# Kernel tuning notes

Measured on AMD Instinct MI355X. Metric: run time of the kernel, lower is better.

Reference implementation:

```python
import jax, jax.numpy as jnp
import numpy as np

D_MODEL, D_INNER, D_STATE, DT_RANK, USERS = 2560, 5120, 16, 160, 32

def setup_inputs() -> dict:
    key = jax.random.key(0)
    ks = jax.random.split(key, 16)
    s = lambda k, shp, sc=0.02: (jax.random.normal(k, shp, dtype=jnp.float32) * sc)
    return {
        "x": jax.random.normal(ks[0], (1, 1, USERS, D_MODEL), dtype=jnp.float32),
        "w_in_ssm": s(ks[1], (D_MODEL, D_INNER)),
        "w_in_mlp": s(ks[2], (D_MODEL, D_INNER)),
        "w_out": s(ks[3], (D_INNER, D_MODEL)),
        "conv_w": s(ks[4], (4, D_INNER), 0.5),
        "conv_b": s(ks[5], (D_INNER,), 0.1),
        "conv_state1": jax.random.normal(ks[6], (1, 1, USERS, D_INNER), dtype=jnp.float32),
        "conv_state2": jax.random.normal(ks[7], (1, 1, USERS, D_INNER), dtype=jnp.float32),
        "conv_state3": jax.random.normal(ks[8], (1, 1, USERS, D_INNER), dtype=jnp.float32),
        "x_proj_w": s(ks[9], (D_INNER, DT_RANK + 2 * D_STATE)),
        "dt_proj_w": s(ks[10], (DT_RANK, D_INNER)),
        "dt_proj_b": s(ks[11], (D_INNER,), 0.1),
        "A_log": jax.random.uniform(ks[12], (D_INNER, D_STATE), dtype=jnp.float32),
        "D_param": s(ks[13], (D_INNER,), 1.0),
        "ssm_state": jax.random.normal(ks[14], (USERS, D_INNER, D_STATE), dtype=jnp.float32) * 0.1,
    }

def reference(x, w_in_ssm, w_in_mlp, w_out, conv_w, conv_b,
              conv_state1, conv_state2, conv_state3,
              x_proj_w, dt_proj_w, dt_proj_b, A_log, D_param, ssm_state):
    xb = x.reshape(USERS, D_MODEL)                       # [U, d_model]
    xs = xb @ w_in_ssm                                    # [U, d_inner] (newest conv tap)
    # 4-tap depthwise causal conv via shifted state buffer (unrolled in original)
    taps = (conv_state1.reshape(USERS, D_INNER),
            conv_state2.reshape(USERS, D_INNER),
            conv_state3.reshape(USERS, D_INNER),
            xs)
    c = taps[0] * conv_w[0] + taps[1] * conv_w[1] + taps[2] * conv_w[2] + taps[3] * conv_w[3] + conv_b
    c = jax.nn.silu(c)                                    # [U, d_inner]
    # selective SSM single-step update
    x_dbl = c @ x_proj_w                                  # [U, dt_rank + 2*d_state]
    dt = jax.nn.softplus(x_dbl[:, :DT_RANK] @ dt_proj_w + dt_proj_b)   # [U, d_inner]
    B = x_dbl[:, DT_RANK:DT_RANK + D_STATE]               # [U, d_state]
    C = x_dbl[:, DT_RANK + D_STATE:]                      # [U, d_state]
    A = -jnp.exp(A_log)                                   # [d_inner, d_state]
    dA = jnp.exp(dt[:, :, None] * A[None])                # [U, d_inner, d_state]
    new_state = ssm_state * dA + (dt * c)[:, :, None] * B[:, None, :]
    y = jnp.einsum("uds,us->ud", new_state, C) + D_param * c           # [U, d_inner]
    res = xb @ w_in_mlp                                   # gate branch (no extra silu, per source)
    out = (y * res) @ w_out                               # [U, d_model]
    return out.reshape(1, 1, USERS, D_MODEL)
```

## Files before the change

kernel.cpp:

```cpp
#include <hip/hip_runtime.h>
#include <hip/hip_bf16.h>
#include <cstdint>
#include <cstddef>

#define U   32
#define DM  2560
#define DI  5120
#define DS  16
#define RNK 160
#define XD  192
#define KC1 8
#define KC4 32

typedef __attribute__((ext_vector_type(8)))  short bf16x8;
typedef __attribute__((ext_vector_type(16))) float f32x16;

__device__ __forceinline__ unsigned int pkbf(float a, float b) {
  __hip_bfloat162 h = __float22bfloat162_rn(make_float2(a, b));
  union { __hip_bfloat162 h; unsigned int u; } v; v.h = h; return v.u;
}
__device__ __forceinline__ unsigned short f2bfu(float f) {
  __hip_bfloat16 h = __float2bfloat16(f);
  union { __hip_bfloat16 h; unsigned short u; } v; v.h = h; return v.u;
}
__device__ __forceinline__ float bf2f(unsigned int s) {
  union { float f; unsigned int u; } v; v.u = s << 16; return v.f;
}

__device__ __forceinline__ void gl_lds16(const float* g, float* l) {
  __builtin_amdgcn_global_load_lds(
      (const __attribute__((address_space(1))) unsigned int*)g,
      (__attribute__((address_space(3))) unsigned int*)l,
      16, 0, 0);
}

template<int LDW, int SLAB>
__global__ __launch_bounds__(256, 3) void skinny_dma(
    const float* __restrict__ A, int lda,
    const float* __restrict__ W0, const float* __restrict__ W1,
    unsigned short* __restrict__ part)
{
  constexpr int NS = SLAB / 16;
  __shared__ float        wbuf[2][16][256];
  __shared__ unsigned int albuf[NS][64][4];

  const int tid  = threadIdx.x;
  const int lane = tid & 63, w = tid >> 6;
  const int kcb  = blockIdx.y, z = blockIdx.z;
  const int k0   = kcb * SLAB;
  const float* __restrict__ W = z ? W1 : W0;
  const int col0 = blockIdx.x * 256;

  for (int i = tid; i < U * (SLAB / 2); i += 256) {
    const int u  = i / (SLAB / 2);
    const int kp = i - u * (SLAB / 2);
    const int k  = 2 * kp;
    const float2 v = *(const float2*)&A[(size_t)u * lda + k0 + k];
    albuf[k >> 4][u + U * ((k >> 3) & 1)][(k >> 1) & 3] = pkbf(v.x, v.y);
  }

  const int cl = lane & 31, half = lane >> 5;

  {
    const float* src = W + ((size_t)k0 + w * 4) * LDW + col0 + lane * 4;
#pragma unroll
    for (int i = 0; i < 4; ++i)
      gl_lds16(src + (size_t)i * LDW, &wbuf[0][w * 4 + i][0]);
  }

  f32x16 acc0{}, acc1{};

  for (int s = 0; s < NS; ++s) {
    const int buf = s & 1;
    if (s + 1 < NS) {
      const float* src = W + ((size_t)k0 + (s + 1) * 16 + w * 4) * LDW
                         + col0 + lane * 4;
#pragma unroll
      for (int i = 0; i < 4; ++i)
        gl_lds16(src + (size_t)i * LDW, &wbuf[buf ^ 1][w * 4 + i][0]);
    }
    __syncthreads();

    bf16x8 af = *(const bf16x8*)&albuf[s][lane][0];
#pragma unroll
    for (int f = 0; f < 2; ++f) {
      const int col = w * 64 + f * 32 + cl;
      float r0 = wbuf[buf][half * 8 + 0][col];
      float r1 = wbuf[buf][half * 8 + 1][col];
      float r2 = wbuf[buf][half * 8 + 2][col];
      float r3 = wbuf[buf][half * 8 + 3][col];
      float r4 = wbuf[buf][half * 8 + 4][col];
      float r5 = wbuf[buf][half * 8 + 5][col];
      float r6 = wbuf[buf][half * 8 + 6][col];
      float r7 = wbuf[buf][half * 8 + 7][col];
      union { bf16x8 v; unsigned int d[4]; } bu;
      bu.d[0] = pkbf(r0, r1); bu.d[1] = pkbf(r2, r3);
      bu.d[2] = pkbf(r4, r5); bu.d[3] = pkbf(r6, r7);
      if (f == 0) acc0 = __builtin_amdgcn_mfma_f32_32x32x16_bf16(af, bu.v, acc0, 0, 0, 0);
      else        acc1 = __builtin_amdgcn_mfma_f32_32x32x16_bf16(af, bu.v, acc1, 0, 0, 0);
    }
    __syncthreads();
  }

  unsigned short* po = part + (size_t)(z * gridDim.y + kcb) * U * LDW + col0;
#pragma unroll
  for (int f = 0; f < 2; ++f) {
    const f32x16& a = f ? acc1 : acc0;
    const int gc = w * 64 + f * 32 + cl;
#pragma unroll
    for (int r = 0; r < 16; ++r) {
      const int m = (r & 3) + 8 * (r >> 2) + 4 * half;
      po[(size_t)m * LDW + gc] = f2bfu(a[r]);
    }
  }
}

__global__ __launch_bounds__(256) void k2a_convsilu(
    const unsigned short* __restrict__ part,
    const float* __restrict__ cs1, const float* __restrict__ cs2,
    const float* __restrict__ cs3,
    const float* __restrict__ cw,  const float* __restrict__ cb,
    float* __restrict__ c_ws, float* __restrict__ res_ws)
{
  const int t = blockIdx.x * 256 + threadIdx.x;
  const int i = 2 * t;
  const int u = i / DI, d = i - u * DI;
  float xs0 = 0.f, xs1 = 0.f, rs0 = 0.f, rs1 = 0.f;
#pragma unroll
  for (int kc = 0; kc < KC1; ++kc) {
    unsigned int a = *(const unsigned int*)&part[((size_t)kc * U + u) * DI + d];
    unsigned int b = *(const unsigned int*)&part[((size_t)(KC1 + kc) * U + u) * DI + d];
    xs0 += bf2f(a & 0xffffu); xs1 += bf2f(a >> 16);
    rs0 += bf2f(b & 0xffffu); rs1 += bf2f(b >> 16);
  }
  const float2 s1 = *(const float2*)&cs1[i];
  const float2 s2 = *(const float2*)&cs2[i];
  const float2 s3 = *(const float2*)&cs3[i];
  const float2 w0 = *(const float2*)&cw[d];
  const float2 w1 = *(const float2*)&cw[DI + d];
  const float2 w2 = *(const float2*)&cw[2 * DI + d];
  const float2 w3 = *(const float2*)&cw[3 * DI + d];
  const float2 bb = *(const float2*)&cb[d];
  float c0 = s1.x * w0.x + s2.x * w1.x + s3.x * w2.x + xs0 * w3.x + bb.x;
  float c1 = s1.y * w0.y + s2.y * w1.y + s3.y * w2.y + xs1 * w3.y + bb.y;
  c0 = c0 / (1.f + __expf(-c0));
  c1 = c1 / (1.f + __expf(-c1));
  *(float2*)&c_ws[i]   = make_float2(c0, c1);
  *(float2*)&res_ws[i] = make_float2(rs0, rs1);
}

__global__ __launch_bounds__(256) void k2b_xproj(
    const float* __restrict__ c_ws,
    const float* __restrict__ xpw,
    float* __restrict__ x_dbl)
{
  __shared__ union { float ct[U][80]; float red[4][64][33]; } sh;
  const int k0 = blockIdx.y * 80;

  for (int i4 = threadIdx.x; i4 < U * 20; i4 += 256) {
    int u = i4 / 20, k4 = i4 - u * 20;
    *(float4*)&sh.ct[u][k4 * 4] = *(const float4*)&c_ws[u * DI + k0 + k4 * 4];
  }
  __syncthreads();

  const int c = threadIdx.x & 63, s = threadIdx.x >> 6;
  const int col = blockIdx.x * 64 + c;
  const float* Wp = xpw + (size_t)(k0 + s * 20) * XD + col;

  float acc[U];
#pragma unroll
  for (int u = 0; u < U; ++u) acc[u] = 0.f;

  for (int kk = 0; kk < 20; kk += 4) {
    float w0 = Wp[(size_t)(kk + 0) * XD];
    float w1 = Wp[(size_t)(kk + 1) * XD];
    float w2 = Wp[(size_t)(kk + 2) * XD];
    float w3 = Wp[(size_t)(kk + 3) * XD];
#pragma unroll
    for (int u = 0; u < U; ++u) {
      float4 cv = *(const float4*)&sh.ct[u][s * 20 + kk];
      acc[u] = fmaf(cv.x, w0, acc[u]);
      acc[u] = fmaf(cv.y, w1, acc[u]);
      acc[u] = fmaf(cv.z, w2, acc[u]);
      acc[u] = fmaf(cv.w, w3, acc[u]);
    }
  }

  __syncthreads();
#pragma unroll
  for (int u = 0; u < U; ++u) sh.red[s][c][u] = acc[u];
  __syncthreads();

  for (int p = threadIdx.x; p < 64 * U; p += 256) {
    int cc = p & 63, u = p >> 6;
    float v = sh.red[0][cc][u] + sh.red[1][cc][u] + sh.red[2][cc][u] + sh.red[3][cc][u];
    atomicAdd(&x_dbl[u * XD + blockIdx.x * 64 + cc], v);
  }
}

__global__ __launch_bounds__(256) void k3a_dt(
    const float* __restrict__ x_dbl,
    const float* __restrict__ dpw, const float* __restrict__ dpb,
    float* __restrict__ dt_ws)
{
  __shared__ union { float xt[U][160]; float red[4][64][33]; } sh;

  for (int i4 = threadIdx.x; i4 < U * 40; i4 += 256) {
    int u = i4 / 40, r4 = i4 - u * 40;
    *(float4*)&sh.xt[u][r4 * 4] = *(const float4*)&x_dbl[u * XD + r4 * 4];
  }
  __syncthreads();

  const int c = threadIdx.x & 63, s = threadIdx.x >> 6;
  const int d = blockIdx.x * 64 + c;
  const float* Wp = dpw + (size_t)(s * 40) * DI + d;

  float acc[U];
#pragma unroll
  for (int u = 0; u < U; ++u) acc[u] = 0.f;

  for (int rr = 0; rr < 40; rr += 4) {
    float w0 = Wp[(size_t)(rr + 0) * DI];
    float w1 = Wp[(size_t)(rr + 1) * DI];
    float w2 = Wp[(size_t)(rr + 2) * DI];
    float w3 = Wp[(size_t)(rr + 3) * DI];
#pragma unroll
    for (int u = 0; u < U; ++u) {
      float4 xv = *(const float4*)&sh.xt[u][s * 40 + rr];
      acc[u] = fmaf(xv.x, w0, acc[u]);
      acc[u] = fmaf(xv.y, w1, acc[u]);
      acc[u] = fmaf(xv.z, w2, acc[u]);
      acc[u] = fmaf(xv.w, w3, acc[u]);
    }
  }

  __syncthreads();
#pragma unroll
  for (int u = 0; u < U; ++u) sh.red[s][c][u] = acc[u];
  __syncthreads();

  for (int p = threadIdx.x; p < 64 * U; p += 256) {
    int cc = p & 63, u = p >> 6;
    int dg = blockIdx.x * 64 + cc;
    float pre = sh.red[0][cc][u] + sh.red[1][cc][u] + sh.red[2][cc][u] + sh.red[3][cc][u]
              + dpb[dg];
    float dt = fmaxf(pre, 0.f) + log1pf(expf(-fabsf(pre)));
    dt_ws[u * DI + dg] = dt;
  }
}

__global__ __launch_bounds__(256) void k3b_ssm(
    const float* __restrict__ x_dbl,
    const float* __restrict__ alog, const float* __restrict__ Dp,
    const float* __restrict__ ssm,
    const float* __restrict__ dt_ws,
    const float* __restrict__ c_ws, const float* __restrict__ res_ws,
    float* __restrict__ yr)
{
  const int i = blockIdx.x * 256 + threadIdx.x;
  const int u = i / DI, d = i - u * DI;

  const float dt = dt_ws[i];
  const float cv = c_ws[i];
  const float rv = res_ws[i];
  const float Dv = Dp[d];
  const float dtc = dt * cv;

  float4 B[4], C[4];
#pragma unroll
  for (int q = 0; q < 4; ++q) {
    B[q] = *(const float4*)&x_dbl[u * XD + RNK + q * 4];
    C[q] = *(const float4*)&x_dbl[u * XD + RNK + DS + q * 4];
  }

  const float* st = ssm + ((size_t)u * DI + d) * DS;
  float y = 0.f;
#pragma unroll
  for (int q = 0; q < 4; ++q) {
    float4 al = *(const float4*)&alog[d * DS + q * 4];
    float4 sv = *(const float4*)&st[q * 4];
    y += (sv.x * __expf(dt * -__expf(al.x)) + dtc * B[q].x) * C[q].x;
    y += (sv.y * __expf(dt * -__expf(al.y)) + dtc * B[q].y) * C[q].y;
    y += (sv.z * __expf(dt * -__expf(al.z)) + dtc * B[q].z) * C[q].z;
    y += (sv.w * __expf(dt * -__expf(al.w)) + dtc * B[q].w) * C[q].w;
  }
  y = fmaf(Dv, cv, y);
  yr[i] = y * rv;
}

__global__ __launch_bounds__(256) void k5_reduce(
    const unsigned short* __restrict__ part4,
    float* __restrict__ out)
{
  const int t = blockIdx.x * 256 + threadIdx.x;
  const int i = 2 * t;
  const int u = i / DM, d = i - u * DM;
  float v0 = 0.f, v1 = 0.f;
#pragma unroll
  for (int kc = 0; kc < KC4; ++kc) {
    unsigned int a = *(const unsigned int*)&part4[((size_t)kc * U + u) * DM + d];
    v0 += bf2f(a & 0xffffu);
    v1 += bf2f(a >> 16);
  }
  *(float2*)&out[i] = make_float2(v0, v1);
}

extern "C" void kernel_launch(void* const* d_in, const int* in_sizes, int n_in,
                              void* d_out, int out_size, void* d_ws, size_t ws_size,
                              hipStream_t stream)
{
  const float* x    = (const float*)d_in[0];
  const float* wssm = (const float*)d_in[1];
  const float* wmlp = (const float*)d_in[2];
  const float* wout = (const float*)d_in[3];
  const float* cw   = (const float*)d_in[4];
  const float* cb   = (const float*)d_in[5];
  const float* cs1  = (const float*)d_in[6];
  const float* cs2  = (const float*)d_in[7];
  const float* cs3  = (const float*)d_in[8];
  const float* xpw  = (const float*)d_in[9];
  const float* dpw  = (const float*)d_in[10];
  const float* dpb  = (const float*)d_in[11];
  const float* alog = (const float*)d_in[12];
  const float* Dp   = (const float*)d_in[13];
  const float* ssm  = (const float*)d_in[14];
  float* out = (float*)d_out;

  unsigned short* partb = (unsigned short*)d_ws;
  float* c_ws   = (float*)(partb + (size_t)2 * KC1 * U * DI);
  float* res_ws = c_ws   + (size_t)U * DI;
  float* dt_ws  = res_ws + (size_t)U * DI;
  float* yrb    = dt_ws  + (size_t)U * DI;
  float* x_dbl  = yrb    + (size_t)U * DI;

  (void)hipMemsetAsync(x_dbl, 0, (size_t)U * XD * sizeof(float), stream);

  skinny_dma<DI, 320><<<dim3(20, KC1, 2), 256, 0, stream>>>(x, DM, wssm, wmlp, partb);
  k2a_convsilu<<<320, 256, 0, stream>>>(partb, cs1, cs2, cs3, cw, cb, c_ws, res_ws);
  k2b_xproj<<<dim3(3, 64), 256, 0, stream>>>(c_ws, xpw, x_dbl);
  k3a_dt<<<80, 256, 0, stream>>>(x_dbl, dpw, dpb, dt_ws);
  k3b_ssm<<<640, 256, 0, stream>>>(x_dbl, alog, Dp, ssm, dt_ws, c_ws, res_ws, yrb);
  skinny_dma<DM, 160><<<dim3(10, KC4, 1), 256, 0, stream>>>(yrb, DI, wout, wout, partb);
  k5_reduce<<<160, 256, 0, stream>>>(partb, out);
}
```

Baseline: 82.03 us.

## Fuse dt projection with SSM update and fold x_dbl zeroing into conv kernel

Merges the dt-projection kernel and the SSM step kernel into one kernel, so dt stays in shared memory and B/C are staged once per block instead of going through a global dt buffer. The separate memset of x_dbl is removed, and the zeroing is done inside the conv/silu kernel. Together these cut two launches and the dt round trip through global memory. In exchange, the SSM work now runs on only 80 blocks instead of 640, which reduces parallelism for the state-streaming part. The reduce loop unroll is also reduced to 8.

```diff
diff --git a/kernel.cpp b/kernel.cpp
--- a/kernel.cpp
+++ b/kernel.cpp
@@ -120,9 +120,12 @@
     const float* __restrict__ cs1, const float* __restrict__ cs2,
     const float* __restrict__ cs3,
     const float* __restrict__ cw,  const float* __restrict__ cb,
-    float* __restrict__ c_ws, float* __restrict__ res_ws)
+    float* __restrict__ c_ws, float* __restrict__ res_ws,
+    float* __restrict__ x_dbl)
 {
   const int t = blockIdx.x * 256 + threadIdx.x;
+  if (t < U * XD / 2) *(float2*)&x_dbl[2 * t] = make_float2(0.f, 0.f);
+
   const int i = 2 * t;
   const int u = i / DI, d = i - u * DI;
   float xs0 = 0.f, xs1 = 0.f, rs0 = 0.f, rs1 = 0.f;
@@ -198,21 +201,32 @@
   }
 }
 
-__global__ __launch_bounds__(256) void k3a_dt(
+__global__ __launch_bounds__(256) void k3_fused(
     const float* __restrict__ x_dbl,
     const float* __restrict__ dpw, const float* __restrict__ dpb,
-    float* __restrict__ dt_ws)
+    const float* __restrict__ alog, const float* __restrict__ Dp,
+    const float* __restrict__ ssm,
+    const float* __restrict__ c_ws, const float* __restrict__ res_ws,
+    float* __restrict__ yr)
 {
   __shared__ union { float xt[U][160]; float red[4][64][33]; } sh;
-
-  for (int i4 = threadIdx.x; i4 < U * 40; i4 += 256) {
+  __shared__ float dtl[U][64];
+  __shared__ float bc[U][32];
+
+  const int tid = threadIdx.x, bx = blockIdx.x;
+
+  for (int i4 = tid; i4 < U * 40; i4 += 256) {
     int u = i4 / 40, r4 = i4 - u * 40;
     *(float4*)&sh.xt[u][r4 * 4] = *(const float4*)&x_dbl[u * XD + r4 * 4];
   }
-  __syncthreads();
-
-  const int c = threadIdx.x & 63, s = threadIdx.x >> 6;
-  const int d = blockIdx.x * 64 + c;
+  for (int i = tid; i < U * 32; i += 256) {
+    int u = i >> 5, j = i & 31;
+    bc[u][j] = x_dbl[u * XD + RNK + j];
+  }
+  __syncthreads();
+
+  const int c = tid & 63, s = tid >> 6;
+  const int d = bx * 64 + c;
   const float* Wp = dpw + (size_t)(s * 40) * DI + d;
 
   float acc[U];
@@ -239,53 +253,38 @@
   for (int u = 0; u < U; ++u) sh.red[s][c][u] = acc[u];
   __syncthreads();
 
-  for (int p = threadIdx.x; p < 64 * U; p += 256) {
+  for (int p = tid; p < 64 * U; p += 256) {
     int cc = p & 63, u = p >> 6;
-    int dg = blockIdx.x * 64 + cc;
     float pre = sh.red[0][cc][u] + sh.red[1][cc][u] + sh.red[2][cc][u] + sh.red[3][cc][u]
-              + dpb[dg];
-    float dt = fmaxf(pre, 0.f) + log1pf(expf(-fabsf(pre)));
-    dt_ws[u * DI + dg] = dt;
-  }
-}
-
-__global__ __launch_bounds__(256) void k3b_ssm(
-    const float* __restrict__ x_dbl,
-    const float* __restrict__ alog, const float* __restrict__ Dp,
-    const float* __restrict__ ssm,
-    const float* __restrict__ dt_ws,
-    const float* __restrict__ c_ws, const float* __restrict__ res_ws,
-    float* __restrict__ yr)
-{
-  const int i = blockIdx.x * 256 + threadIdx.x;
-  const int u = i / DI, d = i - u * DI;
-
-  const float dt = dt_ws[i];
-  const float cv = c_ws[i];
-  const float rv = res_ws[i];
-  const float Dv = Dp[d];
-  const float dtc = dt * cv;
-
-  float4 B[4], C[4];
-#pragma unroll
-  for (int q = 0; q < 4; ++q) {
-    B[q] = *(const float4*)&x_dbl[u * XD + RNK + q * 4];
-    C[q] = *(const float4*)&x_dbl[u * XD + RNK + DS + q * 4];
-  }
-
-  const float* st = ssm + ((size_t)u * DI + d) * DS;
-  float y = 0.f;
-#pragma unroll
-  for (int q = 0; q < 4; ++q) {
-    float4 al = *(const float4*)&alog[d * DS + q * 4];
-    float4 sv = *(const float4*)&st[q * 4];
-    y += (sv.x * __expf(dt * -__expf(al.x)) + dtc * B[q].x) * C[q].x;
-    y += (sv.y * __expf(dt * -__expf(al.y)) + dtc * B[q].y) * C[q].y;
-    y += (sv.z * __expf(dt * -__expf(al.z)) + dtc * B[q].z) * C[q].z;
-    y += (sv.w * __expf(dt * -__expf(al.w)) + dtc * B[q].w) * C[q].w;
-  }
-  y = fmaf(Dv, cv, y);
-  yr[i] = y * rv;
+              + dpb[bx * 64 + cc];
+    dtl[u][cc] = fmaxf(pre, 0.f) + log1pf(expf(-fabsf(pre)));
+  }
+  __syncthreads();
+
+  for (int p = tid; p < 64 * U; p += 256) {
+    const int cc = p & 63, u = p >> 6;
+    const int dg = bx * 64 + cc;
+    const int i  = u * DI + dg;
+    const float dt = dtl[u][cc];
+    const float cv = c_ws[i];
+    const float rv = res_ws[i];
+    const float Dv = Dp[dg];
+    const float dtc = dt * cv;
+
+    const float* st = ssm + ((size_t)u * DI + dg) * DS;
+    float y = 0.f;
+#pragma unroll
+    for (int q = 0; q < 4; ++q) {
+      float4 al = *(const float4*)&alog[dg * DS + q * 4];
+      float4 sv = *(const float4*)&st[q * 4];
+      y += (sv.x * __expf(dt * -__expf(al.x)) + dtc * bc[u][q * 4 + 0])      * bc[u][16 + q * 4 + 0];
+      y += (sv.y * __expf(dt * -__expf(al.y)) + dtc * bc[u][q * 4 + 1])      * bc[u][16 + q * 4 + 1];
+      y += (sv.z * __expf(dt * -__expf(al.z)) + dtc * bc[u][q * 4 + 2])      * bc[u][16 + q * 4 + 2];
+      y += (sv.w * __expf(dt * -__expf(al.w)) + dtc * bc[u][q * 4 + 3])      * bc[u][16 + q * 4 + 3];
+    }
+    y = fmaf(Dv, cv, y);
+    yr[i] = y * rv;
+  }
 }
 
 __global__ __launch_bounds__(256) void k5_reduce(
@@ -296,7 +295,7 @@
   const int i = 2 * t;
   const int u = i / DM, d = i - u * DM;
   float v0 = 0.f, v1 = 0.f;
-#pragma unroll
+#pragma unroll 8
   for (int kc = 0; kc < KC4; ++kc) {
     unsigned int a = *(const unsigned int*)&part4[((size_t)kc * U + u) * DM + d];
     v0 += bf2f(a & 0xffffu);
@@ -329,17 +328,13 @@
   unsigned short* partb = (unsigned short*)d_ws;
   float* c_ws   = (float*)(partb + (size_t)2 * KC1 * U * DI);
   float* res_ws = c_ws   + (size_t)U * DI;
-  float* dt_ws  = res_ws + (size_t)U * DI;
-  float* yrb    = dt_ws  + (size_t)U * DI;
+  float* yrb    = res_ws + (size_t)U * DI;
   float* x_dbl  = yrb    + (size_t)U * DI;
 
-  (void)hipMemsetAsync(x_dbl, 0, (size_t)U * XD * sizeof(float), stream);
-
   skinny_dma<DI, 320><<<dim3(20, KC1, 2), 256, 0, stream>>>(x, DM, wssm, wmlp, partb);
-  k2a_convsilu<<<320, 256, 0, stream>>>(partb, cs1, cs2, cs3, cw, cb, c_ws, res_ws);
+  k2a_convsilu<<<320, 256, 0, stream>>>(partb, cs1, cs2, cs3, cw, cb, c_ws, res_ws, x_dbl);
   k2b_xproj<<<dim3(3, 64), 256, 0, stream>>>(c_ws, xpw, x_dbl);
-  k3a_dt<<<80, 256, 0, stream>>>(x_dbl, dpw, dpb, dt_ws);
-  k3b_ssm<<<640, 256, 0, stream>>>(x_dbl, alog, Dp, ssm, dt_ws, c_ws, res_ws, yrb);
+  k3_fused<<<80, 256, 0, stream>>>(x_dbl, dpw, dpb, alog, Dp, ssm, c_ws, res_ws, yrb);
   skinny_dma<DM, 160><<<dim3(10, KC4, 1), 256, 0, stream>>>(yrb, DI, wout, wout, partb);
   k5_reduce<<<160, 256, 0, stream>>>(partb, out);
 }
```

Result: faster. 77.48 us (-5.6%).
